# Kernel tuning notes

Measured on AMD Instinct MI355X. Metric: run time of the kernel, lower is better.

## Reference

```python
import jax, jax.numpy as jnp
import numpy as np

NUM_HEADS = 16
HEAD_DIM = 64
INNER = NUM_HEADS * HEAD_DIM  # 1024
QUERY_DIM = 1024
CONTEXT_DIM = 768
SCALE = HEAD_DIM ** -0.5


def setup_inputs() -> dict:
    key = jax.random.key(0)
    ks = jax.random.split(key, 6)
    B, NQ, NKV = 8, 1024, 2048
    query = jax.random.normal(ks[0], (B, NQ, QUERY_DIM), dtype=jnp.float32)
    context = jax.random.normal(ks[1], (B, NKV, CONTEXT_DIM), dtype=jnp.float32)
    # weights stored as [in, out] (transpose of torch Linear), math-equivalent
    w_q = jax.random.normal(ks[2], (QUERY_DIM, INNER), dtype=jnp.float32) * (QUERY_DIM ** -0.5)
    w_kv = jax.random.normal(ks[3], (CONTEXT_DIM, 2 * INNER), dtype=jnp.float32) * (CONTEXT_DIM ** -0.5)
    w_out = jax.random.normal(ks[4], (INNER, QUERY_DIM), dtype=jnp.float32) * (INNER ** -0.5)
    b_out = jax.random.normal(ks[5], (QUERY_DIM,), dtype=jnp.float32) * 0.01
    return {"query": query, "context": context, "w_q": w_q, "w_kv": w_kv,
            "w_out": w_out, "b_out": b_out}


def reference(query, context, w_q, w_kv, w_out, b_out):
    B, NQ, _ = query.shape
    NKV = context.shape[1]
    q = query @ w_q                              # [B, NQ, INNER]
    kv = context @ w_kv                          # [B, NKV, 2*INNER]
    k, v = jnp.split(kv, 2, axis=-1)
    # reshape to [B, H, N, D]
    q = q.reshape(B, NQ, NUM_HEADS, HEAD_DIM).transpose(0, 2, 1, 3)
    k = k.reshape(B, NKV, NUM_HEADS, HEAD_DIM).transpose(0, 2, 1, 3)
    v = v.reshape(B, NKV, NUM_HEADS, HEAD_DIM).transpose(0, 2, 1, 3)
    scores = jnp.einsum('bhqd,bhkd->bhqk', q, k) * SCALE
    attn = jax.nn.softmax(scores, axis=-1)
    out = jnp.einsum('bhqk,bhkd->bhqd', attn, v)  # [B, H, NQ, D]
    out = out.transpose(0, 2, 1, 3).reshape(B, NQ, INNER)
    return out @ w_out + b_out
```

## Files before the change

### kernel.cpp

```cpp
#include <hip/hip_runtime.h>
#include <stdint.h>

typedef __bf16 bf16_t;
typedef bf16_t bf16x8 __attribute__((ext_vector_type(8)));
typedef float f32x4 __attribute__((ext_vector_type(4)));
typedef float f32x16 __attribute__((ext_vector_type(16)));
typedef unsigned uint32x2_t __attribute__((ext_vector_type(2)));
typedef unsigned uint32x4_t __attribute__((ext_vector_type(4)));

__device__ __forceinline__ unsigned short f2bf(float x) {
    unsigned u = __builtin_bit_cast(unsigned, x);
    u = (u + 0x7FFFu + ((u >> 16) & 1u)) >> 16;
    return (unsigned short)u;
}

__device__ __forceinline__ unsigned pk_bf16(float lo, float hi) {
    unsigned u0 = __builtin_bit_cast(unsigned, lo) + 0x8000u;
    unsigned u1 = __builtin_bit_cast(unsigned, hi) + 0x8000u;
    return __builtin_amdgcn_perm(u1, u0, 0x07060302u);
}

__device__ __forceinline__ void async_load16(const void* g, void* lds) {
    auto* gp = reinterpret_cast<const __attribute__((address_space(1))) uint32_t*>(
        reinterpret_cast<uintptr_t>(g));
    auto* lp = reinterpret_cast<__attribute__((address_space(3))) uint32_t*>(
        reinterpret_cast<uintptr_t>(lds));
    __builtin_amdgcn_global_load_lds(gp, lp, 16, 0, 0);
}

__device__ __forceinline__ void cast8(const float* __restrict__ src,
                                      unsigned short* __restrict__ dst, int i) {
    const float4* s4 = (const float4*)src;
    float4 a = s4[i * 2], b = s4[i * 2 + 1];
    uint4 o;
    o.x = (unsigned)f2bf(a.x) | ((unsigned)f2bf(a.y) << 16);
    o.y = (unsigned)f2bf(a.z) | ((unsigned)f2bf(a.w) << 16);
    o.z = (unsigned)f2bf(b.x) | ((unsigned)f2bf(b.y) << 16);
    o.w = (unsigned)f2bf(b.z) | ((unsigned)f2bf(b.w) << 16);
    ((uint4*)dst)[i] = o;
}

__device__ __forceinline__ void transcast_body(const float* __restrict__ src,
                                               unsigned short* __restrict__ dst,
                                               int K, int N, float scale,
                                               int bx, int by, float (*tile)[33],
                                               int x, int y) {
    int c0 = bx * 32, r0 = by * 32;
    #pragma unroll
    for (int i = 0; i < 32; i += 8)
        tile[y + i][x] = src[(size_t)(r0 + y + i) * N + c0 + x];
    __syncthreads();
    #pragma unroll
    for (int i = 0; i < 32; i += 8)
        dst[(size_t)(c0 + y + i) * K + r0 + x] = f2bf(tile[x][y + i] * scale);
}

__global__ __launch_bounds__(256) void prep(const float* __restrict__ query,
                                            const float* __restrict__ context,
                                            const float* __restrict__ w_q,
                                            const float* __restrict__ w_kv,
                                            const float* __restrict__ w_out,
                                            unsigned short* __restrict__ qin,
                                            unsigned short* __restrict__ cin,
                                            unsigned short* __restrict__ wqT,
                                            unsigned short* __restrict__ wkvT,
                                            unsigned short* __restrict__ woutT,
                                            float qscale) {
    __shared__ float tile[32][33];
    const int blk = blockIdx.x, tid = threadIdx.x;
    const int x = tid & 31, y = tid >> 5;
    if (blk < 4096) {
        cast8(query, qin, blk * 256 + tid);
    } else if (blk < 10240) {
        cast8(context, cin, (blk - 4096) * 256 + tid);
    } else if (blk < 11264) {
        int lb = blk - 10240;
        transcast_body(w_q, wqT, 1024, 1024, qscale, lb & 31, lb >> 5, tile, x, y);
    } else if (blk < 12800) {
        int lb = blk - 11264;
        transcast_body(w_kv, wkvT, 768, 2048, 1.0f, lb & 63, lb >> 6, tile, x, y);
    } else {
        int lb = blk - 12800;
        transcast_body(w_out, woutT, 1024, 1024, 1.0f, lb & 31, lb >> 5, tile, x, y);
    }
}

template <int EPI>
__global__ __launch_bounds__(256) void gemm_bt(const unsigned short* __restrict__ A,
                                               const unsigned short* __restrict__ Bt,
                                               void* __restrict__ Cout,
                                               const float* __restrict__ bias,
                                               int K, int N, int nkt) {
    __shared__ __align__(16) unsigned short lA[2][128 * 64];
    __shared__ __align__(16) unsigned short lB[2][128 * 64];
    const int tid = threadIdx.x;
    const int w = tid >> 6, l = tid & 63;
    const int wm = w >> 1, wn = w & 1;
    const int row0 = blockIdx.y * 128, col0 = blockIdx.x * 128;
    const int lrow = l & 15, lq = l >> 4;
    const int srow = l >> 3;
    const int scol = ((l & 7) ^ srow) * 8;

    f32x4 acc[4][4];
    #pragma unroll
    for (int i = 0; i < 4; ++i)
        #pragma unroll
        for (int j = 0; j < 4; ++j) acc[i][j] = (f32x4)0.f;

    const unsigned short* ga[4];
    const unsigned short* gb[4];
    #pragma unroll
    for (int q = 0; q < 4; ++q) {
        const int r = (w * 4 + q) * 8 + srow;
        ga[q] = A + (size_t)(row0 + r) * K + scol;
        gb[q] = Bt + (size_t)(col0 + r) * K + scol;
    }

    #pragma unroll
    for (int q = 0; q < 4; ++q) {
        async_load16(ga[q], (char*)lA + (w * 4 + q) * 1024);
        async_load16(gb[q], (char*)lB + (w * 4 + q) * 1024);
        ga[q] += 64;
        gb[q] += 64;
    }
    __syncthreads();

    for (int kt = 0; kt < nkt; ++kt) {
        const int bo = (kt & 1) * 16384;
        if (kt + 1 < nkt) {
            const int bn = bo ^ 16384;
            #pragma unroll
            for (int q = 0; q < 4; ++q) {
                async_load16(ga[q], (char*)lA + bn + (w * 4 + q) * 1024);
                async_load16(gb[q], (char*)lB + bn + (w * 4 + q) * 1024);
                ga[q] += 64;
                gb[q] += 64;
            }
        }
        #pragma unroll
        for (int kc = 0; kc < 2; ++kc) {
            const int pc = ((kc * 4 + lq) ^ (lrow & 7)) * 16;
            bf16x8 af[4], bfr[4];
            #pragma unroll
            for (int i = 0; i < 4; ++i)
                af[i] = *(const bf16x8*)((const char*)lA + bo + (wm * 64 + i * 16 + lrow) * 128 + pc);
            #pragma unroll
            for (int j = 0; j < 4; ++j)
                bfr[j] = *(const bf16x8*)((const char*)lB + bo + (wn * 64 + j * 16 + lrow) * 128 + pc);
            #pragma unroll
            for (int i = 0; i < 4; ++i)
                #pragma unroll
                for (int j = 0; j < 4; ++j)
                    acc[i][j] = __builtin_amdgcn_mfma_f32_16x16x32_bf16(af[i], bfr[j],
                                                                        acc[i][j], 0, 0, 0);
        }
        __syncthreads();
    }
    #pragma unroll
    for (int i = 0; i < 4; ++i) {
        const int grow0 = row0 + wm * 64 + i * 16 + lq * 4;
        #pragma unroll
        for (int j = 0; j < 4; ++j) {
            const int gcol = col0 + wn * 64 + j * 16 + lrow;
            #pragma unroll
            for (int r = 0; r < 4; ++r) {
                float v = acc[i][j][r];
                int grow = grow0 + r;
                if (EPI == 0) {
                    ((unsigned short*)Cout)[(size_t)grow * N + gcol] = f2bf(v);
                } else {
                    ((float*)Cout)[(size_t)grow * N + gcol] = v + bias[gcol];
                }
            }
        }
    }
}

__global__ __launch_bounds__(256, 2) void gemm_kv(const unsigned short* __restrict__ A,
                                                  const unsigned short* __restrict__ Bt,
                                                  unsigned short* __restrict__ Kb,
                                                  unsigned short* __restrict__ Vt) {
    __shared__ __align__(16) unsigned short lA[2][128 * 64];
    __shared__ __align__(16) unsigned short lB[2][128 * 64];
    const int tid = threadIdx.x;
    const int w = tid >> 6, l = tid & 63;
    const int wm = w >> 1, wn = w & 1;
    const int row0 = blockIdx.y * 128, col0 = blockIdx.x * 128;
    const int r32 = l & 31, hw = l >> 5;
    const int srow = l >> 3, scol = ((l & 7) ^ srow) * 8;
    const int r7 = r32 & 7;

    f32x16 acc[2][2];
    #pragma unroll
    for (int mi = 0; mi < 2; ++mi)
        #pragma unroll
        for (int ni = 0; ni < 2; ++ni) acc[mi][ni] = (f32x16)0.f;

    const unsigned short* ga = A + (size_t)(row0 + w * 8 + srow) * 768 + scol;
    const unsigned short* gb = Bt + (size_t)(col0 + w * 8 + srow) * 768 + scol;
    const char* lap = (const char*)lA + (wm * 64 + r32) * 128;
    const char* lbp = (const char*)lB + (wn * 64 + r32) * 128;

    #pragma unroll
    for (int q = 0; q < 4; ++q) {
        async_load16(ga + (size_t)q * 32 * 768, (char*)lA + (q * 32 + w * 8) * 128);
        async_load16(gb + (size_t)q * 32 * 768, (char*)lB + (q * 32 + w * 8) * 128);
    }
    ga += 64;
    gb += 64;
    __syncthreads();

    for (int kt = 0; kt < 12; ++kt) {
        const int bo = (kt & 1) * 16384;
        if (kt < 11) {
            const int bn = bo ^ 16384;
            #pragma unroll
            for (int q = 0; q < 4; ++q) {
                async_load16(ga + (size_t)q * 32 * 768, (char*)lA + bn + (q * 32 + w * 8) * 128);
                async_load16(gb + (size_t)q * 32 * 768, (char*)lB + bn + (q * 32 + w * 8) * 128);
            }
            ga += 64;
            gb += 64;
        }
        #pragma unroll
        for (int ks = 0; ks < 4; ++ks) {
            const int off = ((ks * 2 + hw) ^ r7) * 16;
            bf16x8 af[2], bfr[2];
            #pragma unroll
            for (int mi = 0; mi < 2; ++mi)
                af[mi] = *(const bf16x8*)(lap + bo + mi * 32 * 128 + off);
            #pragma unroll
            for (int ni = 0; ni < 2; ++ni)
                bfr[ni] = *(const bf16x8*)(lbp + bo + ni * 32 * 128 + off);
            #pragma unroll
            for (int mi = 0; mi < 2; ++mi)
                #pragma unroll
                for (int ni = 0; ni < 2; ++ni)
                    acc[mi][ni] = __builtin_amdgcn_mfma_f32_32x32x16_bf16(af[mi], bfr[ni],
                                                                          acc[mi][ni], 0, 0, 0);
        }
        __syncthreads();
    }

    if (col0 < 1024) {
        unsigned short* kp = Kb + (size_t)(row0 + wm * 64) * 1024 + col0 + wn * 64 + r32;
        #pragma unroll
        for (int mi = 0; mi < 2; ++mi)
            #pragma unroll
            for (int ni = 0; ni < 2; ++ni)
                #pragma unroll
                for (int reg = 0; reg < 16; ++reg) {
                    int rr = mi * 32 + (reg & 3) + 8 * (reg >> 2) + 4 * hw;
                    kp[(size_t)rr * 1024 + ni * 32] = f2bf(acc[mi][ni][reg]);
                }
    } else {
        const int bb = row0 >> 11;
        const int keybase = (row0 & 2047) + wm * 64 + 4 * hw;
        const int fvbase = col0 - 1024 + wn * 64 + r32;
        unsigned short* vp = Vt + ((size_t)bb * 1024 + fvbase) * 2048 + keybase;
        #pragma unroll
        for (int mi = 0; mi < 2; ++mi)
            #pragma unroll
            for (int ni = 0; ni < 2; ++ni)
                #pragma unroll
                for (int g = 0; g < 4; ++g) {
                    uint2 pk2;
                    pk2.x = pk_bf16(acc[mi][ni][g * 4 + 0], acc[mi][ni][g * 4 + 1]);
                    pk2.y = pk_bf16(acc[mi][ni][g * 4 + 2], acc[mi][ni][g * 4 + 3]);
                    *(uint2*)(vp + (size_t)(ni * 32) * 2048 + mi * 32 + g * 8) = pk2;
                }
    }
}

__global__ __launch_bounds__(256, 5) void attn_fwd(const unsigned short* __restrict__ qb,
                                                   const unsigned short* __restrict__ kb,
                                                   const unsigned short* __restrict__ vt,
                                                   unsigned short* __restrict__ ob) {
    __shared__ __align__(16) unsigned short lK[2][64 * 64];
    __shared__ __align__(16) unsigned short lV[2][64 * 64];
    const int tid = threadIdx.x;
    const int w = tid >> 6, l = tid & 63;
    const int bh = blockIdx.x;
    const int b = bh >> 4, h = bh & 15;
    const int q0 = blockIdx.y * 64;
    const int lrow = l & 15, lq = l >> 4;
    const int srow = l >> 3, scol = ((l & 7) ^ (srow & 7)) * 8;

    bf16x8 bq[2];
    #pragma unroll
    for (int kc = 0; kc < 2; ++kc) {
        int row = b * 1024 + q0 + w * 16 + lrow;
        int col = h * 64 + kc * 32 + lq * 8;
        bq[kc] = *(const bf16x8*)(qb + (size_t)row * 1024 + col);
    }

    f32x4 ot[4];
    f32x4 lfr = (f32x4)0.f;
    #pragma unroll
    for (int dt = 0; dt < 4; ++dt) ot[dt] = (f32x4)0.f;
    bf16x8 one8;
    #pragma unroll
    for (int i = 0; i < 8; ++i) one8[i] = (bf16_t)1.0f;

    const char* kp0 = (const char*)lK + lrow * 128 + ((lq ^ (lrow & 7)) * 16);
    const char* kp1 = (const char*)lK + lrow * 128 + (((4 + lq) ^ (lrow & 7)) * 16);
    const char* vp0 = (const char*)lV + lrow * 128 + ((lq ^ (lrow & 7)) * 16);
    const char* vp1 = (const char*)lV + lrow * 128 + (((4 + lq) ^ (lrow & 7)) * 16);

    const unsigned short* gkp = kb + (size_t)b * 2048 * 1024 + h * 64 +
                                (size_t)(w * 8 + srow) * 1024 + scol;
    const unsigned short* gvp = vt + (size_t)(b * 1024 + h * 64) * 2048 +
                                (size_t)(w * 8 + srow) * 2048 + scol;
    char* lKw0 = (char*)lK + (w * 8) * 128;
    char* lKw1 = (char*)lK + (32 + w * 8) * 128;
    char* lVw0 = (char*)lV + (w * 8) * 128;
    char* lVw1 = (char*)lV + (32 + w * 8) * 128;

    async_load16(gkp, lKw0);
    async_load16(gkp + 32 * 1024, lKw1);
    async_load16(gvp, lVw0);
    async_load16(gvp + 32 * 2048, lVw1);
    gkp += 64 * 1024;
    gvp += 64;
    __syncthreads();

    for (int it = 0; it < 32; ++it) {
        const int bo = (it & 1) * 8192;
        if (it < 31) {
            const int bn = bo ^ 8192;
            async_load16(gkp, lKw0 + bn);
            async_load16(gkp + 32 * 1024, lKw1 + bn);
            async_load16(gvp, lVw0 + bn);
            async_load16(gvp + 32 * 2048, lVw1 + bn);
            gkp += 64 * 1024;
            gvp += 64;
        }

        bf16x8 ka[4][2];
        #pragma unroll
        for (int mt = 0; mt < 4; ++mt) {
            ka[mt][0] = *(const bf16x8*)(kp0 + bo + mt * 2048);
            ka[mt][1] = *(const bf16x8*)(kp1 + bo + mt * 2048);
        }

        unsigned D[4][2];
        __builtin_amdgcn_s_setprio(1);
        #pragma unroll
        for (int mt = 0; mt < 4; ++mt) {
            f32x4 c = (f32x4)0.f;
            c = __builtin_amdgcn_mfma_f32_16x16x32_bf16(ka[mt][0], bq[0], c, 0, 0, 0);
            c = __builtin_amdgcn_mfma_f32_16x16x32_bf16(ka[mt][1], bq[1], c, 0, 0, 0);
            #pragma unroll
            for (int r = 0; r < 4; ++r)
                c[r] = __builtin_amdgcn_exp2f(c[r]);
            D[mt][0] = pk_bf16(c[0], c[1]);
            D[mt][1] = pk_bf16(c[2], c[3]);
        }
        __builtin_amdgcn_s_setprio(0);

        bf16x8 pb[2];
        {
            uint32x4_t pbw[2];
            #pragma unroll
            for (int half = 0; half < 2; ++half) {
                #pragma unroll
                for (int r2 = 0; r2 < 2; ++r2) {
                    uint32x2_t t = __builtin_amdgcn_permlane32_swap(
                        D[half * 2][r2], D[half * 2 + 1][r2], false, false);
                    uint32x2_t z = __builtin_amdgcn_permlane16_swap(t.x, t.y, false, false);
                    pbw[half][r2] = z.x;
                    pbw[half][r2 + 2] = z.y;
                }
            }
            pb[0] = __builtin_bit_cast(bf16x8, pbw[0]);
            pb[1] = __builtin_bit_cast(bf16x8, pbw[1]);
        }

        bf16x8 va[4][2];
        #pragma unroll
        for (int dt = 0; dt < 4; ++dt) {
            va[dt][0] = *(const bf16x8*)(vp0 + bo + dt * 2048);
            va[dt][1] = *(const bf16x8*)(vp1 + bo + dt * 2048);
        }

        __builtin_amdgcn_s_setprio(1);
        lfr = __builtin_amdgcn_mfma_f32_16x16x32_bf16(one8, pb[0], lfr, 0, 0, 0);
        lfr = __builtin_amdgcn_mfma_f32_16x16x32_bf16(one8, pb[1], lfr, 0, 0, 0);
        #pragma unroll
        for (int dt = 0; dt < 4; ++dt) {
            ot[dt] = __builtin_amdgcn_mfma_f32_16x16x32_bf16(va[dt][0], pb[0], ot[dt], 0, 0, 0);
            ot[dt] = __builtin_amdgcn_mfma_f32_16x16x32_bf16(va[dt][1], pb[1], ot[dt], 0, 0, 0);
        }
        __builtin_amdgcn_s_setprio(0);
        __syncthreads();
    }

    {
        float inv = 1.f / lfr[0];
        size_t grow = (size_t)(b * 1024 + q0 + w * 16 + lrow);
        unsigned short* op = ob + grow * 1024 + h * 64 + 4 * lq;
        #pragma unroll
        for (int dt = 0; dt < 4; ++dt) {
            uint2 pk;
            pk.x = pk_bf16(ot[dt][0] * inv, ot[dt][1] * inv);
            pk.y = pk_bf16(ot[dt][2] * inv, ot[dt][3] * inv);
            *(uint2*)(op + 16 * dt) = pk;
        }
    }
}

extern "C" void kernel_launch(void* const* d_in, const int* in_sizes, int n_in,
                              void* d_out, int out_size, void* d_ws, size_t ws_size,
                              hipStream_t stream) {
    const float* query   = (const float*)d_in[0];
    const float* context = (const float*)d_in[1];
    const float* w_q     = (const float*)d_in[2];
    const float* w_kv    = (const float*)d_in[3];
    const float* w_out   = (const float*)d_in[4];
    const float* b_out   = (const float*)d_in[5];
    float* out = (float*)d_out;

    char* p = (char*)d_ws;
    unsigned short* qin   = (unsigned short*)p; p += (size_t)8192 * 1024 * 2;
    unsigned short* cin   = (unsigned short*)p; p += (size_t)16384 * 768 * 2;
    unsigned short* wqT   = (unsigned short*)p; p += (size_t)1024 * 1024 * 2;
    unsigned short* wkvT  = (unsigned short*)p; p += (size_t)2048 * 768 * 2;
    unsigned short* woutT = (unsigned short*)p; p += (size_t)1024 * 1024 * 2;
    unsigned short* qproj = (unsigned short*)p; p += (size_t)8192 * 1024 * 2;
    unsigned short* kbuf  = (unsigned short*)p; p += (size_t)16384 * 1024 * 2;
    unsigned short* vT    = (unsigned short*)p; p += (size_t)16384 * 1024 * 2;
    unsigned short* obuf  = (unsigned short*)p; p += (size_t)8192 * 1024 * 2;

    const float qscale = 0.125f * 1.44269504088896f;

    prep<<<13824, 256, 0, stream>>>(query, context, w_q, w_kv, w_out,
                                    qin, cin, wqT, wkvT, woutT, qscale);
    gemm_bt<0><<<dim3(8, 64), 256, 0, stream>>>(qin, wqT, qproj, nullptr, 1024, 1024, 16);
    gemm_kv<<<dim3(16, 128), 256, 0, stream>>>(cin, wkvT, kbuf, vT);
    attn_fwd<<<dim3(128, 16), 256, 0, stream>>>(qproj, kbuf, vT, obuf);
    gemm_bt<2><<<dim3(8, 64), 256, 0, stream>>>(obuf, woutT, out, b_out, 1024, 1024, 16);
}
```

Before: 333.3 us.

## Merge Q and KV projections into one launch, double attention query tile

The separate Q-projection and KV-projection GEMMs become one kernel launch over 2560 blocks. A blockIdx swizzle interleaves Q tiles and KV tiles across the grid, and gemm_out gets a similar swizzle for cache locality. Each attention block now handles 128 queries, two 16-row sub-tiles per wave, so every K/V tile loaded into LDS is reused twice. This halves attention K/V traffic but raises register pressure, and occupancy is lowered from 5 to 4 waves.

```diff
diff --git a/kernel.cpp b/kernel.cpp
--- a/kernel.cpp
+++ b/kernel.cpp
@@ -85,18 +85,192 @@
     }
 }
 
-template <int EPI>
-__global__ __launch_bounds__(256) void gemm_bt(const unsigned short* __restrict__ A,
-                                               const unsigned short* __restrict__ Bt,
-                                               void* __restrict__ Cout,
-                                               const float* __restrict__ bias,
-                                               int K, int N, int nkt) {
+__global__ __launch_bounds__(256, 2) void gemm_qkv(const unsigned short* __restrict__ Aq,
+                                                   const unsigned short* __restrict__ Bq,
+                                                   unsigned short* __restrict__ Cq,
+                                                   const unsigned short* __restrict__ Akv,
+                                                   const unsigned short* __restrict__ Bkv,
+                                                   unsigned short* __restrict__ Kb,
+                                                   unsigned short* __restrict__ Vt) {
     __shared__ __align__(16) unsigned short lA[2][128 * 64];
     __shared__ __align__(16) unsigned short lB[2][128 * 64];
     const int tid = threadIdx.x;
     const int w = tid >> 6, l = tid & 63;
     const int wm = w >> 1, wn = w & 1;
-    const int row0 = blockIdx.y * 128, col0 = blockIdx.x * 128;
+    const int srow = l >> 3, scol = ((l & 7) ^ srow) * 8;
+
+    const int swz = (blockIdx.x & 7) * 320 + (blockIdx.x >> 3);
+
+    if (swz < 512) {
+        const int row0 = (swz >> 3) * 128, col0 = (swz & 7) * 128;
+        const int lrow = l & 15, lq = l >> 4;
+
+        f32x4 acc[4][4];
+        #pragma unroll
+        for (int i = 0; i < 4; ++i)
+            #pragma unroll
+            for (int j = 0; j < 4; ++j) acc[i][j] = (f32x4)0.f;
+
+        const unsigned short* ga[4];
+        const unsigned short* gb[4];
+        #pragma unroll
+        for (int q = 0; q < 4; ++q) {
+            const int r = (w * 4 + q) * 8 + srow;
+            ga[q] = Aq + (size_t)(row0 + r) * 1024 + scol;
+            gb[q] = Bq + (size_t)(col0 + r) * 1024 + scol;
+        }
+
+        #pragma unroll
+        for (int q = 0; q < 4; ++q) {
+            async_load16(ga[q], (char*)lA + (w * 4 + q) * 1024);
+            async_load16(gb[q], (char*)lB + (w * 4 + q) * 1024);
+            ga[q] += 64;
+            gb[q] += 64;
+        }
+        __syncthreads();
+
+        for (int kt = 0; kt < 16; ++kt) {
+            const int bo = (kt & 1) * 16384;
+            if (kt + 1 < 16) {
+                const int bn = bo ^ 16384;
+                #pragma unroll
+                for (int q = 0; q < 4; ++q) {
+                    async_load16(ga[q], (char*)lA + bn + (w * 4 + q) * 1024);
+                    async_load16(gb[q], (char*)lB + bn + (w * 4 + q) * 1024);
+                    ga[q] += 64;
+                    gb[q] += 64;
+                }
+            }
+            #pragma unroll
+            for (int kc = 0; kc < 2; ++kc) {
+                const int pc = ((kc * 4 + lq) ^ (lrow & 7)) * 16;
+                bf16x8 af[4], bfr[4];
+                #pragma unroll
+                for (int i = 0; i < 4; ++i)
+                    af[i] = *(const bf16x8*)((const char*)lA + bo + (wm * 64 + i * 16 + lrow) * 128 + pc);
+                #pragma unroll
+                for (int j = 0; j < 4; ++j)
+                    bfr[j] = *(const bf16x8*)((const char*)lB + bo + (wn * 64 + j * 16 + lrow) * 128 + pc);
+                #pragma unroll
+                for (int i = 0; i < 4; ++i)
+                    #pragma unroll
+                    for (int j = 0; j < 4; ++j)
+                        acc[i][j] = __builtin_amdgcn_mfma_f32_16x16x32_bf16(af[i], bfr[j],
+                                                                            acc[i][j], 0, 0, 0);
+            }
+            __syncthreads();
+        }
+        #pragma unroll
+        for (int i = 0; i < 4; ++i) {
+            const int grow0 = row0 + wm * 64 + i * 16 + lq * 4;
+            #pragma unroll
+            for (int j = 0; j < 4; ++j) {
+                const int gcol = col0 + wn * 64 + j * 16 + lrow;
+                #pragma unroll
+                for (int r = 0; r < 4; ++r)
+                    Cq[(size_t)(grow0 + r) * 1024 + gcol] = f2bf(acc[i][j][r]);
+            }
+        }
+    } else {
+        const int id = swz - 512;
+        const int row0 = (id >> 4) * 128, col0 = (id & 15) * 128;
+        const int r32 = l & 31, hw = l >> 5;
+        const int r7 = r32 & 7;
+
+        f32x16 acc[2][2];
+        #pragma unroll
+        for (int mi = 0; mi < 2; ++mi)
+            #pragma unroll
+            for (int ni = 0; ni < 2; ++ni) acc[mi][ni] = (f32x16)0.f;
+
+        const unsigned short* ga = Akv + (size_t)(row0 + w * 8 + srow) * 768 + scol;
+        const unsigned short* gb = Bkv + (size_t)(col0 + w * 8 + srow) * 768 + scol;
+        const char* lap = (const char*)lA + (wm * 64 + r32) * 128;
+        const char* lbp = (const char*)lB + (wn * 64 + r32) * 128;
+
+        #pragma unroll
+        for (int q = 0; q < 4; ++q) {
+            async_load16(ga + (size_t)q * 32 * 768, (char*)lA + (q * 32 + w * 8) * 128);
+            async_load16(gb + (size_t)q * 32 * 768, (char*)lB + (q * 32 + w * 8) * 128);
+        }
+        ga += 64;
+        gb += 64;
+        __syncthreads();
+
+        for (int kt = 0; kt < 12; ++kt) {
+            const int bo = (kt & 1) * 16384;
+            if (kt < 11) {
+                const int bn = bo ^ 16384;
+                #pragma unroll
+                for (int q = 0; q < 4; ++q) {
+                    async_load16(ga + (size_t)q * 32 * 768, (char*)lA + bn + (q * 32 + w * 8) * 128);
+                    async_load16(gb + (size_t)q * 32 * 768, (char*)lB + bn + (q * 32 + w * 8) * 128);
+                }
+                ga += 64;
+                gb += 64;
+            }
+            #pragma unroll
+            for (int ks = 0; ks < 4; ++ks) {
+                const int off = ((ks * 2 + hw) ^ r7) * 16;
+                bf16x8 af[2], bfr[2];
+                #pragma unroll
+                for (int mi = 0; mi < 2; ++mi)
+                    af[mi] = *(const bf16x8*)(lap + bo + mi * 32 * 128 + off);
+                #pragma unroll
+                for (int ni = 0; ni < 2; ++ni)
+                    bfr[ni] = *(const bf16x8*)(lbp + bo + ni * 32 * 128 + off);
+                #pragma unroll
+                for (int mi = 0; mi < 2; ++mi)
+                    #pragma unroll
+                    for (int ni = 0; ni < 2; ++ni)
+                        acc[mi][ni] = __builtin_amdgcn_mfma_f32_32x32x16_bf16(af[mi], bfr[ni],
+                                                                              acc[mi][ni], 0, 0, 0);
+            }
+            __syncthreads();
+        }
+
+        if (col0 < 1024) {
+            unsigned short* kp = Kb + (size_t)(row0 + wm * 64) * 1024 + col0 + wn * 64 + r32;
+            #pragma unroll
+            for (int mi = 0; mi < 2; ++mi)
+                #pragma unroll
+                for (int ni = 0; ni < 2; ++ni)
+                    #pragma unroll
+                    for (int reg = 0; reg < 16; ++reg) {
+                        int rr = mi * 32 + (reg & 3) + 8 * (reg >> 2) + 4 * hw;
+                        kp[(size_t)rr * 1024 + ni * 32] = f2bf(acc[mi][ni][reg]);
+                    }
+        } else {
+            const int bb = row0 >> 11;
+            const int keybase = (row0 & 2047) + wm * 64 + 4 * hw;
+            const int fvbase = col0 - 1024 + wn * 64 + r32;
+            unsigned short* vp = Vt + ((size_t)bb * 1024 + fvbase) * 2048 + keybase;
+            #pragma unroll
+            for (int mi = 0; mi < 2; ++mi)
+                #pragma unroll
+                for (int ni = 0; ni < 2; ++ni)
+                    #pragma unroll
+                    for (int g = 0; g < 4; ++g) {
+                        uint2 pk2;
+                        pk2.x = pk_bf16(acc[mi][ni][g * 4 + 0], acc[mi][ni][g * 4 + 1]);
+                        pk2.y = pk_bf16(acc[mi][ni][g * 4 + 2], acc[mi][ni][g * 4 + 3]);
+                        *(uint2*)(vp + (size_t)(ni * 32) * 2048 + mi * 32 + g * 8) = pk2;
+                    }
+        }
+    }
+}
+
+__global__ __launch_bounds__(256) void gemm_out(const unsigned short* __restrict__ A,
+                                                const unsigned short* __restrict__ Bt,
+                                                float* __restrict__ Cout,
+                                                const float* __restrict__ bias) {
+    __shared__ __align__(16) unsigned short lA[2][128 * 64];
+    __shared__ __align__(16) unsigned short lB[2][128 * 64];
+    const int tid = threadIdx.x;
+    const int w = tid >> 6, l = tid & 63;
+    const int wm = w >> 1, wn = w & 1;
+    const int swz = (blockIdx.x & 7) * 64 + (blockIdx.x >> 3);
+    const int row0 = (swz >> 3) * 128, col0 = (swz & 7) * 128;
     const int lrow = l & 15, lq = l >> 4;
     const int srow = l >> 3;
     const int scol = ((l & 7) ^ srow) * 8;
@@ -112,8 +286,8 @@
     #pragma unroll
     for (int q = 0; q < 4; ++q) {
         const int r = (w * 4 + q) * 8 + srow;
-        ga[q] = A + (size_t)(row0 + r) * K + scol;
-        gb[q] = Bt + (size_t)(col0 + r) * K + scol;
+        ga[q] = A + (size_t)(row0 + r) * 1024 + scol;
+        gb[q] = Bt + (size_t)(col0 + r) * 1024 + scol;
     }
 
     #pragma unroll
@@ -125,9 +299,9 @@
     }
     __syncthreads();
 
-    for (int kt = 0; kt < nkt; ++kt) {
+    for (int kt = 0; kt < 16; ++kt) {
         const int bo = (kt & 1) * 16384;
-        if (kt + 1 < nkt) {
+        if (kt + 1 < 16) {
             const int bn = bo ^ 16384;
             #pragma unroll
             for (int q = 0; q < 4; ++q) {
@@ -163,116 +337,13 @@
         for (int j = 0; j < 4; ++j) {
             const int gcol = col0 + wn * 64 + j * 16 + lrow;
             #pragma unroll
-            for (int r = 0; r < 4; ++r) {
-                float v = acc[i][j][r];
-                int grow = grow0 + r;
-                if (EPI == 0) {
-                    ((unsigned short*)Cout)[(size_t)grow * N + gcol] = f2bf(v);
-                } else {
-                    ((float*)Cout)[(size_t)grow * N + gcol] = v + bias[gcol];
-                }
-            }
-        }
-    }
-}
-
-__global__ __launch_bounds__(256, 2) void gemm_kv(const unsigned short* __restrict__ A,
-                                                  const unsigned short* __restrict__ Bt,
-                                                  unsigned short* __restrict__ Kb,
-                                                  unsigned short* __restrict__ Vt) {
-    __shared__ __align__(16) unsigned short lA[2][128 * 64];
-    __shared__ __align__(16) unsigned short lB[2][128 * 64];
-    const int tid = threadIdx.x;
-    const int w = tid >> 6, l = tid & 63;
-    const int wm = w >> 1, wn = w & 1;
-    const int row0 = blockIdx.y * 128, col0 = blockIdx.x * 128;
-    const int r32 = l & 31, hw = l >> 5;
-    const int srow = l >> 3, scol = ((l & 7) ^ srow) * 8;
-    const int r7 = r32 & 7;
-
-    f32x16 acc[2][2];
-    #pragma unroll
-    for (int mi = 0; mi < 2; ++mi)
-        #pragma unroll
-        for (int ni = 0; ni < 2; ++ni) acc[mi][ni] = (f32x16)0.f;
-
-    const unsigned short* ga = A + (size_t)(row0 + w * 8 + srow) * 768 + scol;
-    const unsigned short* gb = Bt + (size_t)(col0 + w * 8 + srow) * 768 + scol;
-    const char* lap = (const char*)lA + (wm * 64 + r32) * 128;
-    const char* lbp = (const char*)lB + (wn * 64 + r32) * 128;
-
-    #pragma unroll
-    for (int q = 0; q < 4; ++q) {
-        async_load16(ga + (size_t)q * 32 * 768, (char*)lA + (q * 32 + w * 8) * 128);
-        async_load16(gb + (size_t)q * 32 * 768, (char*)lB + (q * 32 + w * 8) * 128);
-    }
-    ga += 64;
-    gb += 64;
-    __syncthreads();
-
-    for (int kt = 0; kt < 12; ++kt) {
-        const int bo = (kt & 1) * 16384;
-        if (kt < 11) {
-            const int bn = bo ^ 16384;
-            #pragma unroll
-            for (int q = 0; q < 4; ++q) {
-                async_load16(ga + (size_t)q * 32 * 768, (char*)lA + bn + (q * 32 + w * 8) * 128);
-                async_load16(gb + (size_t)q * 32 * 768, (char*)lB + bn + (q * 32 + w * 8) * 128);
-            }
-            ga += 64;
-            gb += 64;
-        }
-        #pragma unroll
-        for (int ks = 0; ks < 4; ++ks) {
-            const int off = ((ks * 2 + hw) ^ r7) * 16;
-            bf16x8 af[2], bfr[2];
-            #pragma unroll
-            for (int mi = 0; mi < 2; ++mi)
-                af[mi] = *(const bf16x8*)(lap + bo + mi * 32 * 128 + off);
-            #pragma unroll
-            for (int ni = 0; ni < 2; ++ni)
-                bfr[ni] = *(const bf16x8*)(lbp + bo + ni * 32 * 128 + off);
-            #pragma unroll
-            for (int mi = 0; mi < 2; ++mi)
-                #pragma unroll
-                for (int ni = 0; ni < 2; ++ni)
-                    acc[mi][ni] = __builtin_amdgcn_mfma_f32_32x32x16_bf16(af[mi], bfr[ni],
-                                                                          acc[mi][ni], 0, 0, 0);
-        }
-        __syncthreads();
-    }
-
-    if (col0 < 1024) {
-        unsigned short* kp = Kb + (size_t)(row0 + wm * 64) * 1024 + col0 + wn * 64 + r32;
-        #pragma unroll
-        for (int mi = 0; mi < 2; ++mi)
-            #pragma unroll
-            for (int ni = 0; ni < 2; ++ni)
-                #pragma unroll
-                for (int reg = 0; reg < 16; ++reg) {
-                    int rr = mi * 32 + (reg & 3) + 8 * (reg >> 2) + 4 * hw;
-                    kp[(size_t)rr * 1024 + ni * 32] = f2bf(acc[mi][ni][reg]);
-                }
-    } else {
-        const int bb = row0 >> 11;
-        const int keybase = (row0 & 2047) + wm * 64 + 4 * hw;
-        const int fvbase = col0 - 1024 + wn * 64 + r32;
-        unsigned short* vp = Vt + ((size_t)bb * 1024 + fvbase) * 2048 + keybase;
-        #pragma unroll
-        for (int mi = 0; mi < 2; ++mi)
-            #pragma unroll
-            for (int ni = 0; ni < 2; ++ni)
-                #pragma unroll
-                for (int g = 0; g < 4; ++g) {
-                    uint2 pk2;
-                    pk2.x = pk_bf16(acc[mi][ni][g * 4 + 0], acc[mi][ni][g * 4 + 1]);
-                    pk2.y = pk_bf16(acc[mi][ni][g * 4 + 2], acc[mi][ni][g * 4 + 3]);
-                    *(uint2*)(vp + (size_t)(ni * 32) * 2048 + mi * 32 + g * 8) = pk2;
-                }
-    }
-}
-
-__global__ __launch_bounds__(256, 5) void attn_fwd(const unsigned short* __restrict__ qb,
+            for (int r = 0; r < 4; ++r)
+                Cout[(size_t)(grow0 + r) * 1024 + gcol] = acc[i][j][r] + bias[gcol];
+        }
+    }
+}
+
+__global__ __launch_bounds__(256, 4) void attn_fwd(const unsigned short* __restrict__ qb,
                                                    const unsigned short* __restrict__ kb,
                                                    const unsigned short* __restrict__ vt,
                                                    unsigned short* __restrict__ ob) {
@@ -282,22 +353,28 @@
     const int w = tid >> 6, l = tid & 63;
     const int bh = blockIdx.x;
     const int b = bh >> 4, h = bh & 15;
-    const int q0 = blockIdx.y * 64;
+    const int q0 = blockIdx.y * 128;
     const int lrow = l & 15, lq = l >> 4;
     const int srow = l >> 3, scol = ((l & 7) ^ (srow & 7)) * 8;
 
-    bf16x8 bq[2];
-    #pragma unroll
-    for (int kc = 0; kc < 2; ++kc) {
-        int row = b * 1024 + q0 + w * 16 + lrow;
-        int col = h * 64 + kc * 32 + lq * 8;
-        bq[kc] = *(const bf16x8*)(qb + (size_t)row * 1024 + col);
-    }
-
-    f32x4 ot[4];
-    f32x4 lfr = (f32x4)0.f;
-    #pragma unroll
-    for (int dt = 0; dt < 4; ++dt) ot[dt] = (f32x4)0.f;
+    bf16x8 bq[2][2];
+    #pragma unroll
+    for (int u = 0; u < 2; ++u)
+        #pragma unroll
+        for (int kc = 0; kc < 2; ++kc) {
+            int row = b * 1024 + q0 + w * 32 + u * 16 + lrow;
+            int col = h * 64 + kc * 32 + lq * 8;
+            bq[u][kc] = *(const bf16x8*)(qb + (size_t)row * 1024 + col);
+        }
+
+    f32x4 ot[2][4];
+    f32x4 lfr[2];
+    #pragma unroll
+    for (int u = 0; u < 2; ++u) {
+        #pragma unroll
+        for (int dt = 0; dt < 4; ++dt) ot[u][dt] = (f32x4)0.f;
+        lfr[u] = (f32x4)0.f;
+    }
     bf16x8 one8;
     #pragma unroll
     for (int i = 0; i < 8; ++i) one8[i] = (bf16_t)1.0f;
@@ -343,37 +420,41 @@
             ka[mt][1] = *(const bf16x8*)(kp1 + bo + mt * 2048);
         }
 
-        unsigned D[4][2];
+        unsigned D[2][4][2];
         __builtin_amdgcn_s_setprio(1);
         #pragma unroll
-        for (int mt = 0; mt < 4; ++mt) {
-            f32x4 c = (f32x4)0.f;
-            c = __builtin_amdgcn_mfma_f32_16x16x32_bf16(ka[mt][0], bq[0], c, 0, 0, 0);
-            c = __builtin_amdgcn_mfma_f32_16x16x32_bf16(ka[mt][1], bq[1], c, 0, 0, 0);
-            #pragma unroll
-            for (int r = 0; r < 4; ++r)
-                c[r] = __builtin_amdgcn_exp2f(c[r]);
-            D[mt][0] = pk_bf16(c[0], c[1]);
-            D[mt][1] = pk_bf16(c[2], c[3]);
+        for (int u = 0; u < 2; ++u) {
+            #pragma unroll
+            for (int mt = 0; mt < 4; ++mt) {
+                f32x4 c = (f32x4)0.f;
+                c = __builtin_amdgcn_mfma_f32_16x16x32_bf16(ka[mt][0], bq[u][0], c, 0, 0, 0);
+                c = __builtin_amdgcn_mfma_f32_16x16x32_bf16(ka[mt][1], bq[u][1], c, 0, 0, 0);
+                #pragma unroll
+                for (int r = 0; r < 4; ++r)
+                    c[r] = __builtin_amdgcn_exp2f(c[r]);
+                D[u][mt][0] = pk_bf16(c[0], c[1]);
+                D[u][mt][1] = pk_bf16(c[2], c[3]);
+            }
         }
         __builtin_amdgcn_s_setprio(0);
 
-        bf16x8 pb[2];
-        {
+        bf16x8 pb[2][2];
+        #pragma unroll
+        for (int u = 0; u < 2; ++u) {
             uint32x4_t pbw[2];
             #pragma unroll
             for (int half = 0; half < 2; ++half) {
                 #pragma unroll
                 for (int r2 = 0; r2 < 2; ++r2) {
                     uint32x2_t t = __builtin_amdgcn_permlane32_swap(
-                        D[half * 2][r2], D[half * 2 + 1][r2], false, false);
+                        D[u][half * 2][r2], D[u][half * 2 + 1][r2], false, false);
                     uint32x2_t z = __builtin_amdgcn_permlane16_swap(t.x, t.y, false, false);
                     pbw[half][r2] = z.x;
                     pbw[half][r2 + 2] = z.y;
                 }
             }
-            pb[0] = __builtin_bit_cast(bf16x8, pbw[0]);
-            pb[1] = __builtin_bit_cast(bf16x8, pbw[1]);
+            pb[u][0] = __builtin_bit_cast(bf16x8, pbw[0]);
+            pb[u][1] = __builtin_bit_cast(bf16x8, pbw[1]);
         }
 
         bf16x8 va[4][2];
@@ -384,26 +465,30 @@
         }
 
         __builtin_amdgcn_s_setprio(1);
-        lfr = __builtin_amdgcn_mfma_f32_16x16x32_bf16(one8, pb[0], lfr, 0, 0, 0);
-        lfr = __builtin_amdgcn_mfma_f32_16x16x32_bf16(one8, pb[1], lfr, 0, 0, 0);
-        #pragma unroll
-        for (int dt = 0; dt < 4; ++dt) {
-            ot[dt] = __builtin_amdgcn_mfma_f32_16x16x32_bf16(va[dt][0], pb[0], ot[dt], 0, 0, 0);
-            ot[dt] = __builtin_amdgcn_mfma_f32_16x16x32_bf16(va[dt][1], pb[1], ot[dt], 0, 0, 0);
+        #pragma unroll
+        for (int u = 0; u < 2; ++u) {
+            lfr[u] = __builtin_amdgcn_mfma_f32_16x16x32_bf16(one8, pb[u][0], lfr[u], 0, 0, 0);
+            lfr[u] = __builtin_amdgcn_mfma_f32_16x16x32_bf16(one8, pb[u][1], lfr[u], 0, 0, 0);
+            #pragma unroll
+            for (int dt = 0; dt < 4; ++dt) {
+                ot[u][dt] = __builtin_amdgcn_mfma_f32_16x16x32_bf16(va[dt][0], pb[u][0], ot[u][dt], 0, 0, 0);
+                ot[u][dt] = __builtin_amdgcn_mfma_f32_16x16x32_bf16(va[dt][1], pb[u][1], ot[u][dt], 0, 0, 0);
+            }
         }
         __builtin_amdgcn_s_setprio(0);
         __syncthreads();
     }
 
-    {
-        float inv = 1.f / lfr[0];
-        size_t grow = (size_t)(b * 1024 + q0 + w * 16 + lrow);
+    #pragma unroll
+    for (int u = 0; u < 2; ++u) {
+        float inv = 1.f / lfr[u][0];
+        size_t grow = (size_t)(b * 1024 + q0 + w * 32 + u * 16 + lrow);
         unsigned short* op = ob + grow * 1024 + h * 64 + 4 * lq;
         #pragma unroll
         for (int dt = 0; dt < 4; ++dt) {
             uint2 pk;
-            pk.x = pk_bf16(ot[dt][0] * inv, ot[dt][1] * inv);
-            pk.y = pk_bf16(ot[dt][2] * inv, ot[dt][3] * inv);
+            pk.x = pk_bf16(ot[u][dt][0] * inv, ot[u][dt][1] * inv);
+            pk.y = pk_bf16(ot[u][dt][2] * inv, ot[u][dt][3] * inv);
             *(uint2*)(op + 16 * dt) = pk;
         }
     }
@@ -435,8 +520,7 @@
 
     prep<<<13824, 256, 0, stream>>>(query, context, w_q, w_kv, w_out,
                                     qin, cin, wqT, wkvT, woutT, qscale);
-    gemm_bt<0><<<dim3(8, 64), 256, 0, stream>>>(qin, wqT, qproj, nullptr, 1024, 1024, 16);
-    gemm_kv<<<dim3(16, 128), 256, 0, stream>>>(cin, wkvT, kbuf, vT);
-    attn_fwd<<<dim3(128, 16), 256, 0, stream>>>(qproj, kbuf, vT, obuf);
-    gemm_bt<2><<<dim3(8, 64), 256, 0, stream>>>(obuf, woutT, out, b_out, 1024, 1024, 16);
-}
+    gemm_qkv<<<2560, 256, 0, stream>>>(qin, wqT, qproj, cin, wkvT, kbuf, vT);
+    attn_fwd<<<dim3(128, 8), 256, 0, stream>>>(qproj, kbuf, vT, obuf);
+    gemm_out<<<512, 256, 0, stream>>>(obuf, woutT, out, b_out);
+}
```

Measured after the change: 335.0 us. No clear change (+0.5%).
